# Performance work log

Measured on AMD Instinct MI355X. Metric: run time of the kernel, lower is better.

The kernel has to match this reference:

```python
import jax, jax.numpy as jnp
import numpy as np

# Sizes
NC, NT, NP = 100000, 300000, 50000   # customers, transactions, products
F, DIMC = 8, 16                      # columns per table, per-column embed dim
D = F * DIMC                         # 128 = proj_dim (lazy SAGEConv in-channels)
L, R = 2, 4                          # gnn layers, relation types
OUT = 10                             # out_channels
EM, EI = 300000, 600000              # edges: customer-makes-transaction, product-in-transaction


def setup_inputs() -> dict:
    key = jax.random.key(0)
    ks = jax.random.split(key, 14)
    s = 0.05
    return {
        "x_c": jax.random.normal(ks[0], (NC, F), jnp.float32),
        "x_t": jax.random.normal(ks[1], (NT, F), jnp.float32),
        "x_p": jax.random.normal(ks[2], (NP, F), jnp.float32),
        # per-table per-column numeric embedders: scalar -> DIMC (w*x + b)
        "W_col": jax.random.normal(ks[3], (3, F, DIMC), jnp.float32) * s,
        "b_col": jax.random.normal(ks[4], (3, F, DIMC), jnp.float32) * s,
        # SAGEConv weights per layer per relation: lin_l (neighbor) and lin_r (root)
        "Wn": jax.random.normal(ks[5], (L, R, D, D), jnp.float32) * s,
        "Wr": jax.random.normal(ks[6], (L, R, D, D), jnp.float32) * s,
        "b_lin": jax.random.normal(ks[7], (L, R, D), jnp.float32) * s,
        "W_out": jax.random.normal(ks[8], (D, OUT), jnp.float32) * s,
        "b_out": jax.random.normal(ks[9], (OUT,), jnp.float32) * s,
        "e_makes_src": jax.random.randint(ks[10], (EM,), 0, NC, jnp.int32),
        "e_makes_dst": jax.random.randint(ks[11], (EM,), 0, NT, jnp.int32),
        "e_in_src": jax.random.randint(ks[12], (EI,), 0, NP, jnp.int32),
        "e_in_dst": jax.random.randint(ks[13], (EI,), 0, NT, jnp.int32),
    }


def _embed(x, W, b):
    # x: [N, F]; W,b: [F, DIMC] -> [N, F*DIMC] (concat of per-column embeddings)
    n = x.shape[0]
    return (x[:, :, None] * W[None] + b[None]).reshape(n, -1)


def _sage(x_src, x_dst, src, dst, Wn, Wr, b, n_dst):
    # SAGEConv(mean): out = mean_neigh(x_src) @ Wn + b + x_dst @ Wr
    msg = jax.ops.segment_sum(x_src[src], dst, num_segments=n_dst)
    cnt = jax.ops.segment_sum(jnp.ones(src.shape[0], x_src.dtype), dst, num_segments=n_dst)
    mean = msg / jnp.maximum(cnt, 1.0)[:, None]  # isolated nodes -> 0 message
    return mean @ Wn + x_dst @ Wr + b


def reference(x_c, x_t, x_p, W_col, b_col, Wn, Wr, b_lin, W_out, b_out,
              e_makes_src, e_makes_dst, e_in_src, e_in_dst):
    h_c = _embed(x_c, W_col[0], b_col[0])
    h_t = _embed(x_t, W_col[1], b_col[1])
    h_p = _embed(x_p, W_col[2], b_col[2])
    for l in range(L):
        # R0: customer -makes-> transaction
        o_t0 = _sage(h_c, h_t, e_makes_src, e_makes_dst, Wn[l, 0], Wr[l, 0], b_lin[l, 0], NT)
        # R1: transaction -rev_makes-> customer
        o_c = _sage(h_t, h_c, e_makes_dst, e_makes_src, Wn[l, 1], Wr[l, 1], b_lin[l, 1], NC)
        # R2: product -in-> transaction
        o_t2 = _sage(h_p, h_t, e_in_src, e_in_dst, Wn[l, 2], Wr[l, 2], b_lin[l, 2], NT)
        # R3: transaction -rev_in-> product
        o_p = _sage(h_t, h_p, e_in_dst, e_in_src, Wn[l, 3], Wr[l, 3], b_lin[l, 3], NP)
        # HeteroConv(aggr='mean'): mean over relations targeting each dst type
        h_c, h_t, h_p = o_c, 0.5 * (o_t0 + o_t2), o_p
    logits = h_t @ W_out + b_out  # target_table = 'transaction'
    return jax.nn.softmax(logits, axis=1)
```

## Files before the change

### kernel.cpp

```cpp
#include <hip/hip_runtime.h>

#define NCV 100000
#define NTV 300000
#define NPV 50000
#define OUTC 10
#define EMV 300000
#define EIV 600000
#define YST 16

__global__ __launch_bounds__(256) void fold_heads(
    const float* __restrict__ Wcol, const float* __restrict__ bcol,
    const float* __restrict__ Wn, const float* __restrict__ Wr,
    const float* __restrict__ b_lin, const float* __restrict__ Wout,
    const float* __restrict__ bout,
    int* __restrict__ heads, int nheads, float* __restrict__ B) {
  int tid = threadIdx.x;
  if (blockIdx.x >= 10) {
    int i = (blockIdx.x - 10) * 256 + tid;
    int stride = (gridDim.x - 10) * 256;
    for (; i < nheads; i += stride) heads[i] = -1;
    return;
  }
  __shared__ float sWo[128];
  __shared__ float sT[3][128];
  __shared__ float sQ[7][128];
  const int o = blockIdx.x;
  if (tid < 128) sWo[tid] = Wout[tid * 10 + o];
  __syncthreads();

  const float* Wn00 = Wn;               const float* Wn01 = Wn + 16384;
  const float* Wn02 = Wn + 2 * 16384;   const float* Wn03 = Wn + 3 * 16384;
  const float* Wn10 = Wn + 4 * 16384;   const float* Wn12 = Wn + 6 * 16384;
  const float* Wr00 = Wr;               const float* Wr01 = Wr + 16384;
  const float* Wr02 = Wr + 2 * 16384;   const float* Wr03 = Wr + 3 * 16384;
  const float* Wr10 = Wr + 4 * 16384;   const float* Wr12 = Wr + 6 * 16384;

  for (int task = tid; task < 384; task += 256) {
    int mat = task >> 7, n = task & 127;
    float acc = 0.f;
    if (mat == 0) {
      const float4* w = (const float4*)(Wn10 + n * 128);
      for (int m = 0; m < 32; ++m) {
        float4 w4 = w[m];
        acc += w4.x * sWo[4 * m] + w4.y * sWo[4 * m + 1] +
               w4.z * sWo[4 * m + 2] + w4.w * sWo[4 * m + 3];
      }
    } else if (mat == 1) {
      const float4* w = (const float4*)(Wn12 + n * 128);
      for (int m = 0; m < 32; ++m) {
        float4 w4 = w[m];
        acc += w4.x * sWo[4 * m] + w4.y * sWo[4 * m + 1] +
               w4.z * sWo[4 * m + 2] + w4.w * sWo[4 * m + 3];
      }
    } else {
      const float4* wa = (const float4*)(Wr10 + n * 128);
      const float4* wb = (const float4*)(Wr12 + n * 128);
      for (int m = 0; m < 32; ++m) {
        float4 a = wa[m], b = wb[m];
        acc += 0.5f * ((a.x + b.x) * sWo[4 * m] + (a.y + b.y) * sWo[4 * m + 1] +
                       (a.z + b.z) * sWo[4 * m + 2] + (a.w + b.w) * sWo[4 * m + 3]);
      }
    }
    sT[mat][n] = acc;
  }
  __syncthreads();

  for (int task = tid; task < 896; task += 256) {
    int q = task / 128, k = task & 127;
    const float* Tc = sT[q < 2 ? 0 : (q < 4 ? 1 : 2)];
    const float4* w; const float4* w2 = nullptr;
    switch (q) {
      case 0: w = (const float4*)(Wn01 + k * 128); break;
      case 1: w = (const float4*)(Wr01 + k * 128); break;
      case 2: w = (const float4*)(Wn03 + k * 128); break;
      case 3: w = (const float4*)(Wr03 + k * 128); break;
      case 4: w = (const float4*)(Wn00 + k * 128); break;
      case 5: w = (const float4*)(Wn02 + k * 128); break;
      default: w = (const float4*)(Wr00 + k * 128); w2 = (const float4*)(Wr02 + k * 128); break;
    }
    float acc = 0.f;
    for (int n = 0; n < 32; ++n) {
      float4 w4 = w[n];
      if (w2) { float4 b = w2[n]; w4.x += b.x; w4.y += b.y; w4.z += b.z; w4.w += b.w; }
      acc += w4.x * Tc[4 * n] + w4.y * Tc[4 * n + 1] +
             w4.z * Tc[4 * n + 2] + w4.w * Tc[4 * n + 3];
    }
    sQ[q][k] = acc;
  }
  __syncthreads();

  if (tid < 45) {
    int r = tid;
    const float* WcC = Wcol, *WcT = Wcol + 128, *WcP = Wcol + 256;
    const float* bC = bcol, *bT = bcol + 128, *bP = bcol + 256;
    const float* b00 = b_lin, *b01 = b_lin + 128, *b02 = b_lin + 256, *b03 = b_lin + 384;
    const float* b10 = b_lin + 512, *b12 = b_lin + 768;
    float s = 0.f;
    if (r < 8) {
      for (int j = 0; j < 16; ++j) s += WcT[r * 16 + j] * sQ[0][r * 16 + j];
    } else if (r < 16) {
      int jr = r - 8;
      for (int j = 0; j < 16; ++j)
        s += WcC[jr * 16 + j] * (sQ[1][jr * 16 + j] + sQ[4][jr * 16 + j]);
    } else if (r == 16) {
      for (int k = 0; k < 128; ++k) s += bT[k] * sQ[0][k];
    } else if (r < 25) {
      int jr = r - 17;
      for (int j = 0; j < 16; ++j) s += WcT[jr * 16 + j] * sQ[2][jr * 16 + j];
    } else if (r < 33) {
      int jr = r - 25;
      for (int j = 0; j < 16; ++j)
        s += WcP[jr * 16 + j] * (sQ[3][jr * 16 + j] + sQ[5][jr * 16 + j]);
    } else if (r == 33) {
      for (int k = 0; k < 128; ++k) s += bT[k] * sQ[2][k];
    } else if (r < 42) {
      int jr = r - 34;
      for (int j = 0; j < 16; ++j) s += WcT[jr * 16 + j] * sQ[6][jr * 16 + j];
    } else if (r == 42) {
      for (int k = 0; k < 128; ++k)
        s += bC[k] * (sQ[1][k] + sQ[4][k]) + b01[k] * sT[0][k];
    } else if (r == 43) {
      for (int k = 0; k < 128; ++k)
        s += bP[k] * (sQ[3][k] + sQ[5][k]) + b03[k] * sT[1][k];
    } else {
      for (int n = 0; n < 128; ++n)
        s += (b10[n] + b12[n]) * sWo[n] + bT[n] * sQ[6][n] + (b00[n] + b02[n]) * sT[2][n];
    }
    float v = s * 0.5f;
    if (r == 44) v += bout[o];
    B[r * 10 + o] = v;
  }
}

__global__ __launch_bounds__(256) void build_cp(
    const int* __restrict__ ems, const int* __restrict__ emd,
    const int* __restrict__ eis, const int* __restrict__ eid,
    int* __restrict__ head_c, int* __restrict__ head_p,
    int2* __restrict__ nxt2_mc, int2* __restrict__ nxt2_ip) {
  int g = blockIdx.x * 256 + threadIdx.x;
  if (g >= EIV / 4) return;
  int e0 = g * 4;
  if (g < EMV / 4) {
    int4 s = ((const int4*)ems)[g];
    int4 d = ((const int4*)emd)[g];
    int4 o0, o1;
    o0.x = atomicExch(&head_c[s.x], e0);     o0.y = d.x;
    o0.z = atomicExch(&head_c[s.y], e0 + 1); o0.w = d.y;
    o1.x = atomicExch(&head_c[s.z], e0 + 2); o1.y = d.z;
    o1.z = atomicExch(&head_c[s.w], e0 + 3); o1.w = d.w;
    ((int4*)nxt2_mc)[2 * g] = o0; ((int4*)nxt2_mc)[2 * g + 1] = o1;
  }
  {
    int4 s = ((const int4*)eis)[g];
    int4 d = ((const int4*)eid)[g];
    int4 o0, o1;
    o0.x = atomicExch(&head_p[s.x], e0);     o0.y = d.x;
    o0.z = atomicExch(&head_p[s.y], e0 + 1); o0.w = d.y;
    o1.x = atomicExch(&head_p[s.z], e0 + 2); o1.y = d.z;
    o1.z = atomicExch(&head_p[s.w], e0 + 3); o1.w = d.w;
    ((int4*)nxt2_ip)[2 * g] = o0; ((int4*)nxt2_ip)[2 * g + 1] = o1;
  }
}

__global__ __launch_bounds__(256) void gather_y_buildt(
    const float* __restrict__ xt,
    const int* __restrict__ ems, const int* __restrict__ emd,
    const int* __restrict__ eis, const int* __restrict__ eid,
    const int* __restrict__ head_c, const int* __restrict__ head_p,
    const int2* __restrict__ nxt2_mc, const int2* __restrict__ nxt2_ip,
    int* __restrict__ head_tm, int* __restrict__ head_ti,
    int2* __restrict__ nxt2_mt, int2* __restrict__ nxt2_it,
    const float* __restrict__ xc, const float* __restrict__ xp,
    const float* __restrict__ B,
    float* __restrict__ y_c, float* __restrict__ y_p) {
  __shared__ float sB[340];
  int tid = threadIdx.x;
  for (int i = tid; i < 340; i += 256) sB[i] = B[i];
  int g = blockIdx.x * 256 + tid;

  if (g < EMV / 4) {
    int e0 = g * 4;
    int4 s = ((const int4*)ems)[g];
    int4 d = ((const int4*)emd)[g];
    int4 o0, o1;
    o0.x = atomicExch(&head_tm[d.x], e0);     o0.y = s.x;
    o0.z = atomicExch(&head_tm[d.y], e0 + 1); o0.w = s.y;
    o1.x = atomicExch(&head_tm[d.z], e0 + 2); o1.y = s.z;
    o1.z = atomicExch(&head_tm[d.w], e0 + 3); o1.w = s.w;
    ((int4*)nxt2_mt)[2 * g] = o0; ((int4*)nxt2_mt)[2 * g + 1] = o1;
  }
  if (g < EIV / 4) {
    int e0 = g * 4;
    int4 s = ((const int4*)eis)[g];
    int4 d = ((const int4*)eid)[g];
    int4 o0, o1;
    o0.x = atomicExch(&head_ti[d.x], e0);     o0.y = s.x;
    o0.z = atomicExch(&head_ti[d.y], e0 + 1); o0.w = s.y;
    o1.x = atomicExch(&head_ti[d.z], e0 + 2); o1.y = s.z;
    o1.z = atomicExch(&head_ti[d.w], e0 + 3); o1.w = s.w;
    ((int4*)nxt2_it)[2 * g] = o0; ((int4*)nxt2_it)[2 * g + 1] = o1;
  }
  __syncthreads();

  int i = g;
  if (i >= NCV + NPV) return;
  bool isC = i < NCV;
  int idx = isC ? i : i - NCV;
  const int2* nxt2 = isC ? nxt2_mc : nxt2_ip;
  int e = isC ? head_c[idx] : head_p[idx];

  float acc[8] = {0.f, 0.f, 0.f, 0.f, 0.f, 0.f, 0.f, 0.f};
  float cnt = 0.f;
  while (e >= 0) {
    int2 v = nxt2[e];
    const float4* xr = (const float4*)(xt + (size_t)v.y * 8);
    float4 u = xr[0], w = xr[1];
    acc[0] += u.x; acc[1] += u.y; acc[2] += u.z; acc[3] += u.w;
    acc[4] += w.x; acc[5] += w.y; acc[6] += w.z; acc[7] += w.w;
    cnt += 1.f;
    e = v.x;
  }

  const float* xo = (isC ? xc : xp) + (size_t)idx * 8;
  const float* Bs = sB + (isC ? 0 : 170);
  float gg = cnt > 0.f ? 1.f : 0.f;
  float inv = gg / fmaxf(cnt, 1.f);
  float lg[OUTC];
  #pragma unroll
  for (int o = 0; o < OUTC; ++o) lg[o] = gg * Bs[16 * 10 + o];
  #pragma unroll
  for (int r = 0; r < 8; ++r) {
    float zb = acc[r] * inv;
    float zo = xo[r];
    #pragma unroll
    for (int o = 0; o < OUTC; ++o)
      lg[o] += zb * Bs[r * 10 + o] + zo * Bs[(8 + r) * 10 + o];
  }
  float* y = (isC ? y_c : y_p) + (size_t)idx * YST;
  #pragma unroll
  for (int o = 0; o < OUTC; ++o) y[o] = lg[o];
}

__global__ __launch_bounds__(256) void gather_t(
    const float* __restrict__ y_c, const float* __restrict__ y_p,
    const float* __restrict__ xt,
    const int* __restrict__ head_tm, const int* __restrict__ head_ti,
    const int2* __restrict__ nxt2_mt, const int2* __restrict__ nxt2_it,
    const float* __restrict__ B, float* __restrict__ out) {
  __shared__ float sB[110];
  int tid = threadIdx.x;
  for (int i = tid; i < 110; i += 256) sB[i] = B[340 + i];
  __syncthreads();
  int t = blockIdx.x * 256 + tid;
  if (t >= NTV) return;

  float sc[OUTC] = {0.f, 0.f, 0.f, 0.f, 0.f, 0.f, 0.f, 0.f, 0.f, 0.f};
  float sp[OUTC] = {0.f, 0.f, 0.f, 0.f, 0.f, 0.f, 0.f, 0.f, 0.f, 0.f};
  float dc = 0.f, dp = 0.f;
  int e1 = head_tm[t], e2 = head_ti[t];
  while (e1 >= 0 || e2 >= 0) {
    if (e1 >= 0) {
      int2 v = nxt2_mt[e1];
      const float* yr = y_c + (size_t)v.y * YST;
      float4 u = *(const float4*)yr;
      float4 w = *(const float4*)(yr + 4);
      float2 z = *(const float2*)(yr + 8);
      sc[0] += u.x; sc[1] += u.y; sc[2] += u.z; sc[3] += u.w;
      sc[4] += w.x; sc[5] += w.y; sc[6] += w.z; sc[7] += w.w;
      sc[8] += z.x; sc[9] += z.y;
      dc += 1.f;
      e1 = v.x;
    }
    if (e2 >= 0) {
      int2 v = nxt2_it[e2];
      const float* yr = y_p + (size_t)v.y * YST;
      float4 u = *(const float4*)yr;
      float4 w = *(const float4*)(yr + 4);
      float2 z = *(const float2*)(yr + 8);
      sp[0] += u.x; sp[1] += u.y; sp[2] += u.z; sp[3] += u.w;
      sp[4] += w.x; sp[5] += w.y; sp[6] += w.z; sp[7] += w.w;
      sp[8] += z.x; sp[9] += z.y;
      dp += 1.f;
      e2 = v.x;
    }
  }

  float Gc = dc > 0.f ? 1.f : 0.f, Gp = dp > 0.f ? 1.f : 0.f;
  float ivc = 1.f / fmaxf(dc, 1.f), ivp = 1.f / fmaxf(dp, 1.f);

  const float4* xp4 = (const float4*)(xt + (size_t)t * 8);
  float4 xa = xp4[0], xb = xp4[1];
  float xv[8] = {xa.x, xa.y, xa.z, xa.w, xb.x, xb.y, xb.z, xb.w};

  float lg[OUTC];
  #pragma unroll
  for (int o = 0; o < OUTC; ++o)
    lg[o] = sc[o] * ivc + sp[o] * ivp +
            Gc * sB[80 + o] + Gp * sB[90 + o] + sB[100 + o];
  #pragma unroll
  for (int r = 0; r < 8; ++r) {
    float xr = xv[r];
    #pragma unroll
    for (int o = 0; o < OUTC; ++o) lg[o] += xr * sB[r * 10 + o];
  }

  float m = lg[0];
  #pragma unroll
  for (int o = 1; o < OUTC; ++o) m = fmaxf(m, lg[o]);
  float s = 0.f;
  #pragma unroll
  for (int o = 0; o < OUTC; ++o) { lg[o] = __expf(lg[o] - m); s += lg[o]; }
  float invs = 1.0f / s;
  float* op = &out[(size_t)t * OUTC];
  #pragma unroll
  for (int o = 0; o < 5; ++o) {
    float2 p2; p2.x = lg[2 * o] * invs; p2.y = lg[2 * o + 1] * invs;
    *(float2*)&op[2 * o] = p2;
  }
}

extern "C" void kernel_launch(void* const* d_in, const int* in_sizes, int n_in,
                              void* d_out, int out_size, void* d_ws, size_t ws_size,
                              hipStream_t stream) {
  const float* x_c   = (const float*)d_in[0];
  const float* x_t   = (const float*)d_in[1];
  const float* x_p   = (const float*)d_in[2];
  const float* W_col = (const float*)d_in[3];
  const float* b_col = (const float*)d_in[4];
  const float* Wn    = (const float*)d_in[5];
  const float* Wr    = (const float*)d_in[6];
  const float* b_lin = (const float*)d_in[7];
  const float* W_out = (const float*)d_in[8];
  const float* b_out = (const float*)d_in[9];
  const int* e_m_src = (const int*)d_in[10];
  const int* e_m_dst = (const int*)d_in[11];
  const int* e_i_src = (const int*)d_in[12];
  const int* e_i_dst = (const int*)d_in[13];
  float* out = (float*)d_out;

  size_t cursor = 0;
  char* base = (char*)d_ws;
  auto alloc = [&](size_t bytes) {
    void* p = base + cursor;
    cursor += (bytes + 255) & ~(size_t)255;
    return p;
  };
  float* y_c  = (float*)alloc((size_t)NCV * YST * 4);
  float* y_p  = (float*)alloc((size_t)NPV * YST * 4);
  int nheads = NCV + NPV + 2 * NTV;
  int* heads  = (int*)alloc((size_t)nheads * 4);
  int* head_c  = heads;
  int* head_p  = heads + NCV;
  int* head_tm = heads + NCV + NPV;
  int* head_ti = heads + NCV + NPV + NTV;
  int2* nxt2_mc = (int2*)alloc((size_t)EMV * 8);
  int2* nxt2_mt = (int2*)alloc((size_t)EMV * 8);
  int2* nxt2_ip = (int2*)alloc((size_t)EIV * 8);
  int2* nxt2_it = (int2*)alloc((size_t)EIV * 8);
  float* B    = (float*)alloc(450 * 4);

  fold_heads<<<128, 256, 0, stream>>>(
      W_col, b_col, Wn, Wr, b_lin, W_out, b_out, heads, nheads, B);

  build_cp<<<(EIV / 4 + 255) / 256, 256, 0, stream>>>(
      e_m_src, e_m_dst, e_i_src, e_i_dst,
      head_c, head_p, nxt2_mc, nxt2_ip);

  gather_y_buildt<<<(EIV / 4 + 255) / 256, 256, 0, stream>>>(
      x_t, e_m_src, e_m_dst, e_i_src, e_i_dst,
      head_c, head_p, nxt2_mc, nxt2_ip,
      head_tm, head_ti, nxt2_mt, nxt2_it,
      x_c, x_p, B, y_c, y_p);

  gather_t<<<(NTV + 255) / 256, 256, 0, stream>>>(
      y_c, y_p, x_t, head_tm, head_ti, nxt2_mt, nxt2_it, B, out);
}
```

Before: 276.8 us.

## Embed payload in edge records to replace indirect gathers with edge-local reads

After: 294.6 us. 6.4% more time.

```diff
diff --git a/kernel.cpp b/kernel.cpp
--- a/kernel.cpp
+++ b/kernel.cpp
@@ -6,7 +6,9 @@
 #define OUTC 10
 #define EMV 300000
 #define EIV 600000
-#define YST 16
+
+__device__ __forceinline__ float i2f(int v) { return __int_as_float(v); }
+__device__ __forceinline__ int f2i(float v) { return __float_as_int(v); }
 
 __global__ __launch_bounds__(256) void fold_heads(
     const float* __restrict__ Wcol, const float* __restrict__ bcol,
@@ -132,93 +134,70 @@
   }
 }
 
-__global__ __launch_bounds__(256) void build_cp(
+__global__ __launch_bounds__(256) void build_graph(
     const int* __restrict__ ems, const int* __restrict__ emd,
     const int* __restrict__ eis, const int* __restrict__ eid,
+    const float* __restrict__ xt,
     int* __restrict__ head_c, int* __restrict__ head_p,
-    int2* __restrict__ nxt2_mc, int2* __restrict__ nxt2_ip) {
-  int g = blockIdx.x * 256 + threadIdx.x;
-  if (g >= EIV / 4) return;
-  int e0 = g * 4;
-  if (g < EMV / 4) {
-    int4 s = ((const int4*)ems)[g];
-    int4 d = ((const int4*)emd)[g];
-    int4 o0, o1;
-    o0.x = atomicExch(&head_c[s.x], e0);     o0.y = d.x;
-    o0.z = atomicExch(&head_c[s.y], e0 + 1); o0.w = d.y;
-    o1.x = atomicExch(&head_c[s.z], e0 + 2); o1.y = d.z;
-    o1.z = atomicExch(&head_c[s.w], e0 + 3); o1.w = d.w;
-    ((int4*)nxt2_mc)[2 * g] = o0; ((int4*)nxt2_mc)[2 * g + 1] = o1;
-  }
-  {
-    int4 s = ((const int4*)eis)[g];
-    int4 d = ((const int4*)eid)[g];
-    int4 o0, o1;
-    o0.x = atomicExch(&head_p[s.x], e0);     o0.y = d.x;
-    o0.z = atomicExch(&head_p[s.y], e0 + 1); o0.w = d.y;
-    o1.x = atomicExch(&head_p[s.z], e0 + 2); o1.y = d.z;
-    o1.z = atomicExch(&head_p[s.w], e0 + 3); o1.w = d.w;
-    ((int4*)nxt2_ip)[2 * g] = o0; ((int4*)nxt2_ip)[2 * g + 1] = o1;
-  }
-}
-
-__global__ __launch_bounds__(256) void gather_y_buildt(
-    const float* __restrict__ xt,
-    const int* __restrict__ ems, const int* __restrict__ emd,
-    const int* __restrict__ eis, const int* __restrict__ eid,
+    int* __restrict__ head_tm, int* __restrict__ head_ti,
+    int4* __restrict__ cnm, int4* __restrict__ cni) {
+  int e = blockIdx.x * 256 + threadIdx.x;
+  int4 z = make_int4(0, 0, 0, 0);
+  if (e < EMV) {
+    int c = ems[e], t = emd[e];
+    int cn = atomicExch(&head_c[c], e);
+    int tn = atomicExch(&head_tm[t], e);
+    const int4* xr = (const int4*)(xt + (size_t)t * 8);
+    int4 x0 = xr[0], x1 = xr[1];
+    cnm[4 * (size_t)e]     = make_int4(cn, tn, x0.x, x0.y);
+    cnm[4 * (size_t)e + 1] = make_int4(x0.z, x0.w, x1.x, x1.y);
+    cnm[4 * (size_t)e + 2] = make_int4(x1.z, x1.w, 0, 0);
+    cnm[4 * (size_t)e + 3] = z;
+  }
+  if (e < EIV) {
+    int p = eis[e], t = eid[e];
+    int pn = atomicExch(&head_p[p], e);
+    int tn = atomicExch(&head_ti[t], e);
+    const int4* xr = (const int4*)(xt + (size_t)t * 8);
+    int4 x0 = xr[0], x1 = xr[1];
+    cni[4 * (size_t)e]     = make_int4(pn, tn, x0.x, x0.y);
+    cni[4 * (size_t)e + 1] = make_int4(x0.z, x0.w, x1.x, x1.y);
+    cni[4 * (size_t)e + 2] = make_int4(x1.z, x1.w, 0, 0);
+    cni[4 * (size_t)e + 3] = z;
+  }
+}
+
+__global__ __launch_bounds__(256) void gather_y(
     const int* __restrict__ head_c, const int* __restrict__ head_p,
-    const int2* __restrict__ nxt2_mc, const int2* __restrict__ nxt2_ip,
-    int* __restrict__ head_tm, int* __restrict__ head_ti,
-    int2* __restrict__ nxt2_mt, int2* __restrict__ nxt2_it,
+    const int4* __restrict__ cnm, const int4* __restrict__ cni,
     const float* __restrict__ xc, const float* __restrict__ xp,
     const float* __restrict__ B,
-    float* __restrict__ y_c, float* __restrict__ y_p) {
+    int4* __restrict__ tnm, int4* __restrict__ tni) {
   __shared__ float sB[340];
   int tid = threadIdx.x;
   for (int i = tid; i < 340; i += 256) sB[i] = B[i];
-  int g = blockIdx.x * 256 + tid;
-
-  if (g < EMV / 4) {
-    int e0 = g * 4;
-    int4 s = ((const int4*)ems)[g];
-    int4 d = ((const int4*)emd)[g];
-    int4 o0, o1;
-    o0.x = atomicExch(&head_tm[d.x], e0);     o0.y = s.x;
-    o0.z = atomicExch(&head_tm[d.y], e0 + 1); o0.w = s.y;
-    o1.x = atomicExch(&head_tm[d.z], e0 + 2); o1.y = s.z;
-    o1.z = atomicExch(&head_tm[d.w], e0 + 3); o1.w = s.w;
-    ((int4*)nxt2_mt)[2 * g] = o0; ((int4*)nxt2_mt)[2 * g + 1] = o1;
-  }
-  if (g < EIV / 4) {
-    int e0 = g * 4;
-    int4 s = ((const int4*)eis)[g];
-    int4 d = ((const int4*)eid)[g];
-    int4 o0, o1;
-    o0.x = atomicExch(&head_ti[d.x], e0);     o0.y = s.x;
-    o0.z = atomicExch(&head_ti[d.y], e0 + 1); o0.w = s.y;
-    o1.x = atomicExch(&head_ti[d.z], e0 + 2); o1.y = s.z;
-    o1.z = atomicExch(&head_ti[d.w], e0 + 3); o1.w = s.w;
-    ((int4*)nxt2_it)[2 * g] = o0; ((int4*)nxt2_it)[2 * g + 1] = o1;
-  }
-  __syncthreads();
-
-  int i = g;
+  __syncthreads();
+  int i = blockIdx.x * 256 + tid;
   if (i >= NCV + NPV) return;
   bool isC = i < NCV;
   int idx = isC ? i : i - NCV;
-  const int2* nxt2 = isC ? nxt2_mc : nxt2_ip;
-  int e = isC ? head_c[idx] : head_p[idx];
+  const int4* cn = isC ? cnm : cni;
+  int4* tn = isC ? tnm : tni;
+  int head = isC ? head_c[idx] : head_p[idx];
 
   float acc[8] = {0.f, 0.f, 0.f, 0.f, 0.f, 0.f, 0.f, 0.f};
   float cnt = 0.f;
+  int e = head;
   while (e >= 0) {
-    int2 v = nxt2[e];
-    const float4* xr = (const float4*)(xt + (size_t)v.y * 8);
-    float4 u = xr[0], w = xr[1];
-    acc[0] += u.x; acc[1] += u.y; acc[2] += u.z; acc[3] += u.w;
-    acc[4] += w.x; acc[5] += w.y; acc[6] += w.z; acc[7] += w.w;
+    int4 w0 = cn[4 * (size_t)e];
+    int4 w1 = cn[4 * (size_t)e + 1];
+    int4 w2 = cn[4 * (size_t)e + 2];
+    acc[0] += i2f(w0.z); acc[1] += i2f(w0.w);
+    acc[2] += i2f(w1.x); acc[3] += i2f(w1.y);
+    acc[4] += i2f(w1.z); acc[5] += i2f(w1.w);
+    acc[6] += i2f(w2.x); acc[7] += i2f(w2.y);
     cnt += 1.f;
-    e = v.x;
+    e = w0.x;
   }
 
   const float* xo = (isC ? xc : xp) + (size_t)idx * 8;
@@ -236,16 +215,25 @@
     for (int o = 0; o < OUTC; ++o)
       lg[o] += zb * Bs[r * 10 + o] + zo * Bs[(8 + r) * 10 + o];
   }
-  float* y = (isC ? y_c : y_p) + (size_t)idx * YST;
-  #pragma unroll
-  for (int o = 0; o < OUTC; ++o) y[o] = lg[o];
+
+  int4 y1 = make_int4(f2i(lg[3]), f2i(lg[4]), f2i(lg[5]), f2i(lg[6]));
+  int4 y2 = make_int4(f2i(lg[7]), f2i(lg[8]), f2i(lg[9]), 0);
+  int4 z = make_int4(0, 0, 0, 0);
+  e = head;
+  while (e >= 0) {
+    int4 w0 = cn[4 * (size_t)e];
+    tn[4 * (size_t)e]     = make_int4(w0.y, f2i(lg[0]), f2i(lg[1]), f2i(lg[2]));
+    tn[4 * (size_t)e + 1] = y1;
+    tn[4 * (size_t)e + 2] = y2;
+    tn[4 * (size_t)e + 3] = z;
+    e = w0.x;
+  }
 }
 
 __global__ __launch_bounds__(256) void gather_t(
-    const float* __restrict__ y_c, const float* __restrict__ y_p,
+    const int4* __restrict__ tnm, const int4* __restrict__ tni,
     const float* __restrict__ xt,
     const int* __restrict__ head_tm, const int* __restrict__ head_ti,
-    const int2* __restrict__ nxt2_mt, const int2* __restrict__ nxt2_it,
     const float* __restrict__ B, float* __restrict__ out) {
   __shared__ float sB[110];
   int tid = threadIdx.x;
@@ -260,28 +248,24 @@
   int e1 = head_tm[t], e2 = head_ti[t];
   while (e1 >= 0 || e2 >= 0) {
     if (e1 >= 0) {
-      int2 v = nxt2_mt[e1];
-      const float* yr = y_c + (size_t)v.y * YST;
-      float4 u = *(const float4*)yr;
-      float4 w = *(const float4*)(yr + 4);
-      float2 z = *(const float2*)(yr + 8);
-      sc[0] += u.x; sc[1] += u.y; sc[2] += u.z; sc[3] += u.w;
-      sc[4] += w.x; sc[5] += w.y; sc[6] += w.z; sc[7] += w.w;
-      sc[8] += z.x; sc[9] += z.y;
+      int4 w0 = tnm[4 * (size_t)e1];
+      int4 w1 = tnm[4 * (size_t)e1 + 1];
+      int4 w2 = tnm[4 * (size_t)e1 + 2];
+      sc[0] += i2f(w0.y); sc[1] += i2f(w0.z); sc[2] += i2f(w0.w);
+      sc[3] += i2f(w1.x); sc[4] += i2f(w1.y); sc[5] += i2f(w1.z); sc[6] += i2f(w1.w);
+      sc[7] += i2f(w2.x); sc[8] += i2f(w2.y); sc[9] += i2f(w2.z);
       dc += 1.f;
-      e1 = v.x;
+      e1 = w0.x;
     }
     if (e2 >= 0) {
-      int2 v = nxt2_it[e2];
-      const float* yr = y_p + (size_t)v.y * YST;
-      float4 u = *(const float4*)yr;
-      float4 w = *(const float4*)(yr + 4);
-      float2 z = *(const float2*)(yr + 8);
-      sp[0] += u.x; sp[1] += u.y; sp[2] += u.z; sp[3] += u.w;
-      sp[4] += w.x; sp[5] += w.y; sp[6] += w.z; sp[7] += w.w;
-      sp[8] += z.x; sp[9] += z.y;
+      int4 w0 = tni[4 * (size_t)e2];
+      int4 w1 = tni[4 * (size_t)e2 + 1];
+      int4 w2 = tni[4 * (size_t)e2 + 2];
+      sp[0] += i2f(w0.y); sp[1] += i2f(w0.z); sp[2] += i2f(w0.w);
+      sp[3] += i2f(w1.x); sp[4] += i2f(w1.y); sp[5] += i2f(w1.z); sp[6] += i2f(w1.w);
+      sp[7] += i2f(w2.x); sp[8] += i2f(w2.y); sp[9] += i2f(w2.z);
       dp += 1.f;
-      e2 = v.x;
+      e2 = w0.x;
     }
   }
 
@@ -345,33 +329,28 @@
     cursor += (bytes + 255) & ~(size_t)255;
     return p;
   };
-  float* y_c  = (float*)alloc((size_t)NCV * YST * 4);
-  float* y_p  = (float*)alloc((size_t)NPV * YST * 4);
   int nheads = NCV + NPV + 2 * NTV;
   int* heads  = (int*)alloc((size_t)nheads * 4);
   int* head_c  = heads;
   int* head_p  = heads + NCV;
   int* head_tm = heads + NCV + NPV;
   int* head_ti = heads + NCV + NPV + NTV;
-  int2* nxt2_mc = (int2*)alloc((size_t)EMV * 8);
-  int2* nxt2_mt = (int2*)alloc((size_t)EMV * 8);
-  int2* nxt2_ip = (int2*)alloc((size_t)EIV * 8);
-  int2* nxt2_it = (int2*)alloc((size_t)EIV * 8);
-  float* B    = (float*)alloc(450 * 4);
+  int4* cnm = (int4*)alloc((size_t)EMV * 64);
+  int4* cni = (int4*)alloc((size_t)EIV * 64);
+  int4* tnm = (int4*)alloc((size_t)EMV * 64);
+  int4* tni = (int4*)alloc((size_t)EIV * 64);
+  float* B  = (float*)alloc(450 * 4);
 
   fold_heads<<<128, 256, 0, stream>>>(
       W_col, b_col, Wn, Wr, b_lin, W_out, b_out, heads, nheads, B);
 
-  build_cp<<<(EIV / 4 + 255) / 256, 256, 0, stream>>>(
-      e_m_src, e_m_dst, e_i_src, e_i_dst,
-      head_c, head_p, nxt2_mc, nxt2_ip);
-
-  gather_y_buildt<<<(EIV / 4 + 255) / 256, 256, 0, stream>>>(
-      x_t, e_m_src, e_m_dst, e_i_src, e_i_dst,
-      head_c, head_p, nxt2_mc, nxt2_ip,
-      head_tm, head_ti, nxt2_mt, nxt2_it,
-      x_c, x_p, B, y_c, y_p);
+  build_graph<<<(EIV + 255) / 256, 256, 0, stream>>>(
+      e_m_src, e_m_dst, e_i_src, e_i_dst, x_t,
+      head_c, head_p, head_tm, head_ti, cnm, cni);
+
+  gather_y<<<(NCV + NPV + 255) / 256, 256, 0, stream>>>(
+      head_c, head_p, cnm, cni, x_c, x_p, B, tnm, tni);
 
   gather_t<<<(NTV + 255) / 256, 256, 0, stream>>>(
-      y_c, y_p, x_t, head_tm, head_ti, nxt2_mt, nxt2_it, B, out);
-}
+      tnm, tni, x_t, head_tm, head_ti, B, out);
+}
```
